# Kernel optimization log

Hardware: AMD Instinct MI355X
Metric: run time of the kernel (lower is better)

## Reference

```python
import jax, jax.numpy as jnp
import numpy as np

D, B, E, O = 8, 16, 2048, 2048  # delays, batch, pre, post


def setup_inputs() -> dict:
    key = jax.random.key(0)
    k_w, k_mask, k_xd, k_dm, k_ws, k_sp = jax.random.split(key, 6)
    # W = connectivity mask * magnitudes (sparse non-negative weights, buffer wmax folded in)
    conn = jax.random.bernoulli(k_mask, 0.1, (E, O)).astype(jnp.float32)
    W = jax.random.uniform(k_w, (E, O), dtype=jnp.float32) * 0.02 * conn
    # Delayed presynaptic spikes: sparse binary
    Xd = jax.random.bernoulli(k_xd, 0.02, (D, B, E)).astype(jnp.float32)
    # delaymap: binary (delay, pre, post) routing map, typically ~1 active delay per synapse
    delaymap = jax.random.bernoulli(k_dm, 0.125, (D, E, O)).astype(jnp.float32)
    # STP modulation (output of shortterm module, before the +1 offset)
    Wshort = (jax.random.uniform(k_ws, (D, B, E), dtype=jnp.float32) - 0.5) * 0.4
    # Per-presynaptic-neuron signs in {-1,+1}, stored as int
    signs_pre = jax.random.randint(k_sp, (E,), 0, 2, dtype=jnp.int32)
    return {"W": W, "Xd": Xd, "delaymap": delaymap, "Wshort": Wshort,
            "signs_pre": signs_pre}


def reference(W, Xd, delaymap, Wshort, signs_pre):
    # align_signs(): signs = signs_pre broadcast over post, zeroed where W <= 0
    s = (2 * signs_pre - 1).astype(W.dtype)  # map {0,1} -> {-1,+1}
    signs = jnp.where(W > 0, s[:, None], jnp.zeros((), W.dtype))  # (E, O)
    Ws = signs * W  # signed weights 'eo'
    # has_STP path: I = einsum('eo,dbe,deo,dbe->bo', W, Xd, delaymap, Wshort+1)
    I = jnp.einsum('eo,dbe,deo,dbe->bo', Ws, Xd, delaymap, Wshort + 1.0)
    return I
```

## Files before the change

kernel.cpp:

```cpp
#include <hip/hip_runtime.h>


constexpr int D = 8, B = 16, E = 2048, O = 2048;
constexpr int DB = D * B;
constexpr int OTILE = 512;
constexpr int THREADS2 = OTILE / 4;
constexpr int ESPLIT = 4;
constexpr int NSLICE = D * ESPLIT;

struct Entry { int e; float c; };

__global__ __launch_bounds__(256) void build_lists(
    const float* __restrict__ Xd, const float* __restrict__ Wshort,
    const int* __restrict__ signs, int* __restrict__ counts,
    Entry* __restrict__ entries)
{
    const int db = blockIdx.x;
    __shared__ int cnt;
    if (threadIdx.x == 0) cnt = 0;
    __syncthreads();
    const float* xrow = Xd + (size_t)db * E;
    const float* wsr  = Wshort + (size_t)db * E;
    Entry* out = entries + (size_t)db * E;
    for (int e = threadIdx.x; e < E; e += blockDim.x) {
        float x = xrow[e];
        if (x != 0.0f) {
            float s = (float)(2 * signs[e] - 1);
            float c = x * s * (1.0f + wsr[e]);
            int slot = atomicAdd(&cnt, 1);
            out[slot].e = e;
            out[slot].c = c;
        }
    }
    __syncthreads();
    if (threadIdx.x == 0) counts[db] = cnt;
}

__global__ __launch_bounds__(THREADS2) void accum(
    const float* __restrict__ W, const float* __restrict__ dm,
    const int* __restrict__ counts, const Entry* __restrict__ entries,
    float* __restrict__ partial)
{
    const int tile = blockIdx.x;
    const int part = blockIdx.y;
    const int db   = blockIdx.z;
    const int d = db >> 4;
    const int b = db & 15;
    const int o0 = tile * OTILE + (int)threadIdx.x * 4;

    const int n = counts[db];
    const Entry* __restrict__ lst = entries + (size_t)db * E;

    __shared__ Entry sh[E / ESPLIT];
    for (int j = threadIdx.x; part + j * ESPLIT < n; j += THREADS2)
        sh[j] = lst[part + j * ESPLIT];
    const int m = (n - part + ESPLIT - 1) / ESPLIT;
    __syncthreads();

    const float* __restrict__ dmd = dm + (size_t)d * E * O;
    float4 acc = make_float4(0.f, 0.f, 0.f, 0.f);
    #pragma unroll 4
    for (int j = 0; j < m; ++j) {
        Entry en = sh[j];
        const float4 w  = *(const float4*)(W   + (size_t)en.e * O + o0);
        const float4 mm = *(const float4*)(dmd + (size_t)en.e * O + o0);
        acc.x += en.c * w.x * mm.x;
        acc.y += en.c * w.y * mm.y;
        acc.z += en.c * w.z * mm.z;
        acc.w += en.c * w.w * mm.w;
    }

    float* p = partial + ((size_t)(d * ESPLIT + part) * B + b) * O + o0;
    *(float4*)p = acc;
}

__global__ __launch_bounds__(256) void reduce_slices(
    const float* __restrict__ partial, float* __restrict__ Iout)
{
    const int bo = blockIdx.x * 256 + threadIdx.x;
    float s = 0.f;
    #pragma unroll
    for (int k = 0; k < NSLICE; ++k)
        s += partial[(size_t)k * B * O + bo];
    Iout[bo] = s;
}

extern "C" void kernel_launch(void* const* d_in, const int* in_sizes, int n_in,
                              void* d_out, int out_size, void* d_ws, size_t ws_size,
                              hipStream_t stream) {
    const float* W     = (const float*)d_in[0];
    const float* Xd    = (const float*)d_in[1];
    const float* dm    = (const float*)d_in[2];
    const float* Wsh   = (const float*)d_in[3];
    const int*   signs = (const int*)d_in[4];
    float* Iout = (float*)d_out;

    int*   counts  = (int*)d_ws;
    Entry* entries = (Entry*)((char*)d_ws + 512);
    float* partial = (float*)((char*)d_ws + (4u << 20));

    build_lists<<<dim3(DB), dim3(256), 0, stream>>>(Xd, Wsh, signs, counts, entries);
    dim3 grid(O / OTILE, ESPLIT, DB);
    accum<<<grid, dim3(THREADS2), 0, stream>>>(W, dm, counts, entries, partial);
    reduce_slices<<<dim3(B * O / 256), dim3(256), 0, stream>>>(partial, Iout);
}
```

Before: 199.8 us.

## Vectorize list building and reduction, drop LDS staging, halve E split

```diff
diff --git a/kernel.cpp b/kernel.cpp
--- a/kernel.cpp
+++ b/kernel.cpp
@@ -5,7 +5,7 @@
 constexpr int DB = D * B;
 constexpr int OTILE = 512;
 constexpr int THREADS2 = OTILE / 4;
-constexpr int ESPLIT = 4;
+constexpr int ESPLIT = 2;
 constexpr int NSLICE = D * ESPLIT;
 
 struct Entry { int e; float c; };
@@ -19,17 +19,25 @@
     __shared__ int cnt;
     if (threadIdx.x == 0) cnt = 0;
     __syncthreads();
-    const float* xrow = Xd + (size_t)db * E;
-    const float* wsr  = Wshort + (size_t)db * E;
-    Entry* out = entries + (size_t)db * E;
-    for (int e = threadIdx.x; e < E; e += blockDim.x) {
-        float x = xrow[e];
-        if (x != 0.0f) {
-            float s = (float)(2 * signs[e] - 1);
-            float c = x * s * (1.0f + wsr[e]);
-            int slot = atomicAdd(&cnt, 1);
-            out[slot].e = e;
-            out[slot].c = c;
+    const float4* __restrict__ xrow = (const float4*)(Xd + (size_t)db * E);
+    const float4* __restrict__ wsr  = (const float4*)(Wshort + (size_t)db * E);
+    Entry* __restrict__ out = entries + (size_t)db * E;
+    for (int q = threadIdx.x; q < E / 4; q += 256) {
+        float4 x = xrow[q];
+        if (x.x == 0.f && x.y == 0.f && x.z == 0.f && x.w == 0.f) continue;
+        float4 ws = wsr[q];
+        const float xa[4] = {x.x, x.y, x.z, x.w};
+        const float wa[4] = {ws.x, ws.y, ws.z, ws.w};
+        #pragma unroll
+        for (int k = 0; k < 4; ++k) {
+            if (xa[k] != 0.f) {
+                int e = q * 4 + k;
+                float s = (float)(2 * signs[e] - 1);
+                float c = xa[k] * s * (1.0f + wa[k]);
+                int slot = atomicAdd(&cnt, 1);
+                out[slot].e = e;
+                out[slot].c = c;
+            }
         }
     }
     __syncthreads();
@@ -49,21 +57,17 @@
     const int o0 = tile * OTILE + (int)threadIdx.x * 4;
 
     const int n = counts[db];
-    const Entry* __restrict__ lst = entries + (size_t)db * E;
+    const Entry* __restrict__ lst = entries + (size_t)db * E + part;
+    const int m = (n > part) ? ((n - part + ESPLIT - 1) / ESPLIT) : 0;
 
-    __shared__ Entry sh[E / ESPLIT];
-    for (int j = threadIdx.x; part + j * ESPLIT < n; j += THREADS2)
-        sh[j] = lst[part + j * ESPLIT];
-    const int m = (n - part + ESPLIT - 1) / ESPLIT;
-    __syncthreads();
-
-    const float* __restrict__ dmd = dm + (size_t)d * E * O;
+    const float* __restrict__ Wt  = W  + o0;
+    const float* __restrict__ dmd = dm + (size_t)d * E * O + o0;
     float4 acc = make_float4(0.f, 0.f, 0.f, 0.f);
     #pragma unroll 4
     for (int j = 0; j < m; ++j) {
-        Entry en = sh[j];
-        const float4 w  = *(const float4*)(W   + (size_t)en.e * O + o0);
-        const float4 mm = *(const float4*)(dmd + (size_t)en.e * O + o0);
+        Entry en = lst[j * ESPLIT];
+        const float4 w  = *(const float4*)(Wt  + (size_t)en.e * O);
+        const float4 mm = *(const float4*)(dmd + (size_t)en.e * O);
         acc.x += en.c * w.x * mm.x;
         acc.y += en.c * w.y * mm.y;
         acc.z += en.c * w.z * mm.z;
@@ -77,12 +81,15 @@
 __global__ __launch_bounds__(256) void reduce_slices(
     const float* __restrict__ partial, float* __restrict__ Iout)
 {
-    const int bo = blockIdx.x * 256 + threadIdx.x;
-    float s = 0.f;
+    const int q = blockIdx.x * 256 + threadIdx.x;
+    const float4* __restrict__ p = (const float4*)partial;
+    float4 s = make_float4(0.f, 0.f, 0.f, 0.f);
     #pragma unroll
-    for (int k = 0; k < NSLICE; ++k)
-        s += partial[(size_t)k * B * O + bo];
-    Iout[bo] = s;
+    for (int k = 0; k < NSLICE; ++k) {
+        float4 v = p[(size_t)k * (B * O / 4) + q];
+        s.x += v.x; s.y += v.y; s.z += v.z; s.w += v.w;
+    }
+    ((float4*)Iout)[q] = s;
 }
 
 extern "C" void kernel_launch(void* const* d_in, const int* in_sizes, int n_in,
@@ -102,5 +109,5 @@
     build_lists<<<dim3(DB), dim3(256), 0, stream>>>(Xd, Wsh, signs, counts, entries);
     dim3 grid(O / OTILE, ESPLIT, DB);
     accum<<<grid, dim3(THREADS2), 0, stream>>>(W, dm, counts, entries, partial);
-    reduce_slices<<<dim3(B * O / 256), dim3(256), 0, stream>>>(partial, Iout);
+    reduce_slices<<<dim3(B * O / (256 * 4)), dim3(256), 0, stream>>>(partial, Iout);
 }
```

Measured after the change: 196.7 us. Within noise of the previous version (-1.6%).
